# Performance work log

Hardware: AMD Instinct MI355X
Metric: run time of the kernel (lower is better)

Reference implementation:

```python
import jax, jax.numpy as jnp
import numpy as np

S, B, I, H = 2048, 4096, 2, 6  # seq, batch, input_size, hidden_size


def setup_inputs() -> dict:
    key = jax.random.key(0)
    ks = jax.random.split(key, 11)
    init = lambda k, sh: jax.random.normal(k, sh, dtype=jnp.float32) * 0.1
    return {
        "x": jax.random.normal(ks[0], (S, B, I), dtype=jnp.float32),
        # layer-0 LSTM params (PyTorch gate order: i, f, g, o)
        "Wih0": init(ks[1], (4 * H, I)),
        "Whh0": init(ks[2], (4 * H, H)),
        "bih0": init(ks[3], (4 * H,)),
        "bhh0": init(ks[4], (4 * H,)),
        # layer-1 LSTM params
        "Wih1": init(ks[5], (4 * H, H)),
        "Whh1": init(ks[6], (4 * H, H)),
        "bih1": init(ks[7], (4 * H,)),
        "bhh1": init(ks[8], (4 * H,)),
        # final Linear(6, 1)
        "W2": init(ks[9], (1, H)),
        "b2": init(ks[10], (1,)),
    }


def _lstm_layer(x, Wih, Whh, bih, bhh):
    # x: (S, B, in_dim) -> hidden outputs (S, B, H)
    Bn = x.shape[1]
    Hn = Whh.shape[1]
    b = bih + bhh
    # precompute input projections for all timesteps at once (memory-bound GEMM)
    xg = jnp.einsum("sbi,gi->sbg", x, Wih) + b  # (S, B, 4H)

    def step(carry, xt_g):
        h, c = carry
        g = xt_g + h @ Whh.T  # (B, 4H)
        i, f, gg, o = jnp.split(g, 4, axis=-1)
        i = jax.nn.sigmoid(i)
        f = jax.nn.sigmoid(f)
        gg = jnp.tanh(gg)
        o = jax.nn.sigmoid(o)
        c = f * c + i * gg
        h = o * jnp.tanh(c)
        return (h, c), h

    h0 = jnp.zeros((Bn, Hn), dtype=x.dtype)
    c0 = jnp.zeros((Bn, Hn), dtype=x.dtype)
    _, hs = jax.lax.scan(step, (h0, c0), xg)
    return hs  # (S, B, H)


def reference(x, Wih0, Whh0, bih0, bhh0, Wih1, Whh1, bih1, bhh1, W2, b2):
    h1 = _lstm_layer(x, Wih0, Whh0, bih0, bhh0)   # (S, B, H)
    h2 = _lstm_layer(h1, Wih1, Whh1, bih1, bhh1)  # (S, B, H); dropout disabled (eval)
    flat = h2.reshape(-1, H)                       # (S*B, H)
    out = flat @ W2.T + b2                         # (S*B, 1) — original discards final view
    return out
```

## Files before the change

kernel.cpp:

```cpp
#include <hip/hip_runtime.h>

#define SEQ   2048
#define BATCH 4096
#define HID   6
#define BLK   256

typedef float v2f __attribute__((ext_vector_type(2)));
typedef unsigned u2 __attribute__((ext_vector_type(2)));

__device__ __forceinline__ float fexp2(float a) {
#if __has_builtin(__builtin_amdgcn_exp2f)
  return __builtin_amdgcn_exp2f(a);
#else
  float r; asm("v_exp_f32 %0, %1" : "=v"(r) : "v"(a)); return r;
#endif
}
__device__ __forceinline__ float frcp(float a) {
#if __has_builtin(__builtin_amdgcn_rcpf)
  return __builtin_amdgcn_rcpf(a);
#else
  float r; asm("v_rcp_f32 %0, %1" : "=v"(r) : "v"(a)); return r;
#endif
}

template <int CTRL>
__device__ __forceinline__ float dppf(float v) {
  int r = __builtin_amdgcn_update_dpp(0, __builtin_bit_cast(int, v), CTRL, 0xF, 0xF, true);
  return __builtin_bit_cast(float, r);
}

template <int OFF>
__device__ __forceinline__ float swzf(float v) {
  int r = __builtin_amdgcn_ds_swizzle(__builtin_bit_cast(int, v), OFF);
  return __builtin_bit_cast(float, r);
}
#define BC0 0x18
#define BC1 0x38
#define BC2 0x58
#define BC3 0x78
#define BC4 0x98
#define BC5 0xB8

__device__ __forceinline__ float xor16f(float v, bool hi) {
#if __has_builtin(__builtin_amdgcn_permlane16_swap)
  u2 r = __builtin_amdgcn_permlane16_swap(__builtin_bit_cast(unsigned, v),
                                          __builtin_bit_cast(unsigned, v), false, false);
  return __builtin_bit_cast(float, hi ? r.x : r.y);
#else
  unsigned d = __builtin_bit_cast(unsigned, v), s = d;
  asm volatile("v_permlane16_swap_b32 %0, %1" : "+v"(d), "+v"(s));
  return __builtin_bit_cast(float, hi ? d : s);
#endif
}

__global__ __launch_bounds__(BLK, 2) void lstm2_kernel(
    const float* __restrict__ x,
    const float* __restrict__ Wih0, const float* __restrict__ Whh0,
    const float* __restrict__ bih0, const float* __restrict__ bhh0,
    const float* __restrict__ Wih1, const float* __restrict__ Whh1,
    const float* __restrict__ bih1, const float* __restrict__ bhh1,
    const float* __restrict__ W2,   const float* __restrict__ b2,
    float* __restrict__ out)
{
  __shared__ float obuf[64][8];

  const int tid = threadIdx.x;
  const int wib = tid >> 6;
  const int l6  = tid & 63;
  const int el  = l6 >> 5;
  const int r5  = l6 & 31;
  const bool hiL = (r5 & 16) != 0;
  const int p   = (r5 >> 3) & 1;
  const int u   = r5 & 7;
  const int uu  = (u < HID) ? u : (HID - 1);
  const int b   = blockIdx.x * 8 + wib * 2 + el;

  const int r0 = p ? (2 * HID + uu) : uu;
  const int r1 = p ? (3 * HID + uu) : (HID + uu);
  const float A  = p ? 2.f : 1.f;
  const float Bc = p ? -1.f : 0.f;
  const float K0 = p ? -2.8853900817779268f : -1.4426950408889634f;
  const float K1 = -1.4426950408889634f;
  const float KT =  2.8853900817779268f;

  v2f WA0[3], WA1[3], WB0[3], WB1[3];
  float BS0, BS1;
  if (!hiL) {
    WA0[0] = v2f{K0 * Wih0[r0 * 2 + 0], K0 * Wih0[r0 * 2 + 1]};
    WA1[0] = v2f{K1 * Wih0[r1 * 2 + 0], K1 * Wih0[r1 * 2 + 1]};
    WA0[1] = v2f{0.f, 0.f}; WA0[2] = v2f{0.f, 0.f};
    WA1[1] = v2f{0.f, 0.f}; WA1[2] = v2f{0.f, 0.f};
#pragma unroll
    for (int k = 0; k < 3; ++k) {
      WB0[k] = v2f{K0 * Whh0[r0 * HID + 2 * k], K0 * Whh0[r0 * HID + 2 * k + 1]};
      WB1[k] = v2f{K1 * Whh0[r1 * HID + 2 * k], K1 * Whh0[r1 * HID + 2 * k + 1]};
    }
    BS0 = K0 * (bih0[r0] + bhh0[r0]);
    BS1 = K1 * (bih0[r1] + bhh0[r1]);
  } else {
#pragma unroll
    for (int k = 0; k < 3; ++k) {
      WA0[k] = v2f{K0 * Wih1[r0 * HID + 2 * k], K0 * Wih1[r0 * HID + 2 * k + 1]};
      WA1[k] = v2f{K1 * Wih1[r1 * HID + 2 * k], K1 * Wih1[r1 * HID + 2 * k + 1]};
      WB0[k] = v2f{K0 * Whh1[r0 * HID + 2 * k], K0 * Whh1[r0 * HID + 2 * k + 1]};
      WB1[k] = v2f{K1 * Whh1[r1 * HID + 2 * k], K1 * Whh1[r1 * HID + 2 * k + 1]};
    }
    BS0 = K0 * (bih1[r0] + bhh1[r0]);
    BS1 = K1 * (bih1[r1] + bhh1[r1]);
  }
  const v2f w2p0 = v2f{W2[0], W2[1]}, w2p1 = v2f{W2[2], W2[3]}, w2p2 = v2f{W2[4], W2[5]};
  const float bout = b2[0];

  float h = 0.f, c = 0.f;

  auto gath = [&](float hv, v2f (&g)[3]) {
    g[0] = v2f{swzf<BC0>(hv), swzf<BC1>(hv)};
    g[1] = v2f{swzf<BC2>(hv), swzf<BC3>(hv)};
    g[2] = v2f{swzf<BC4>(hv), swzf<BC5>(hv)};
  };

  auto step = [&](v2f xc, float& ov) {
    v2f g2[3]; gath(h, g2);
    float hs = xor16f(h, hiL);
    v2f g1[3]; gath(hs, g1);
    v2f v10 = hiL ? g1[0] : xc;

    v2f a0v = __builtin_elementwise_fma(WA0[0], v10, v2f{BS0, 0.f});
    a0v = __builtin_elementwise_fma(WA0[1], g1[1], a0v);
    a0v = __builtin_elementwise_fma(WA0[2], g1[2], a0v);
    a0v = __builtin_elementwise_fma(WB0[0], g2[0], a0v);
    a0v = __builtin_elementwise_fma(WB0[1], g2[1], a0v);
    a0v = __builtin_elementwise_fma(WB0[2], g2[2], a0v);
    float a0 = a0v.x + a0v.y;

    v2f a1v = __builtin_elementwise_fma(WA1[0], v10, v2f{BS1, 0.f});
    a1v = __builtin_elementwise_fma(WA1[1], g1[1], a1v);
    a1v = __builtin_elementwise_fma(WA1[2], g1[2], a1v);
    a1v = __builtin_elementwise_fma(WB1[0], g2[0], a1v);
    a1v = __builtin_elementwise_fma(WB1[1], g2[1], a1v);
    a1v = __builtin_elementwise_fma(WB1[2], g2[2], a1v);
    float a1 = a1v.x + a1v.y;

    v2f ao = __builtin_elementwise_fma(w2p0, g2[0],
             __builtin_elementwise_fma(w2p1, g2[1],
             __builtin_elementwise_fma(w2p2, g2[2], v2f{bout, 0.f})));
    ov = ao.x + ao.y;

    float g0  = fmaf(A, frcp(1.f + fexp2(a0)), Bc);
    float g1v = frcp(1.f + fexp2(a1));
    float xg0 = dppf<0x128>(g0);
    float xg1 = dppf<0x128>(g1v);
    float m = g0 * xg0;
    float f = p ? xg1 : g1v;
    float o = p ? g1v : xg1;
    c = fmaf(f, c, m);
    float th = fmaf(-2.f, frcp(1.f + fexp2(c * KT)), 1.f);
    h = o * th;
  };

  auto flush = [&](int rbase) {
    const int r = tid >> 2, jj = (tid & 3) * 2;
    float2 vv = *(const float2*)&obuf[r][jj];
    *(float2*)&out[(size_t)(rbase + r) * BATCH + blockIdx.x * 8 + jj] = vv;
  };

  const v2f* x2 = (const v2f*)x;
  v2f xc  = x2[(size_t)0 * BATCH + b];
  v2f xn1 = x2[(size_t)1 * BATCH + b];
  v2f xn2 = x2[(size_t)2 * BATCH + b];
  v2f xn3 = x2[(size_t)3 * BATCH + b];

  {
    float ov;
    step(xc, ov);
    if (hiL) { h = 0.f; c = 0.f; }
    v2f xf = x2[(size_t)4 * BATCH + b];
    xc = xn1; xn1 = xn2; xn2 = xn3; xn3 = xf;
  }

#pragma unroll 1
  for (int t = 1; t < SEQ; ++t) {
    int tf = t + 4; tf = (tf < SEQ) ? tf : (SEQ - 1);
    v2f xf = x2[(size_t)tf * BATCH + b];

    float ov;
    step(xc, ov);

    if (t >= 2) {
      const int r = t - 2;
      if (hiL && p == 0 && u == 0) obuf[r & 63][wib * 2 + el] = ov;
      if ((r & 63) == 63) {
        __syncthreads();
        flush(r - 63);
        __syncthreads();
      }
    }
    xc = xn1; xn1 = xn2; xn2 = xn3; xn3 = xf;
  }

  {
    float ov;
    step(xc, ov);
    if (hiL && p == 0 && u == 0) obuf[62][wib * 2 + el] = ov;
    v2f g2[3]; gath(h, g2);
    v2f ao = __builtin_elementwise_fma(w2p0, g2[0],
             __builtin_elementwise_fma(w2p1, g2[1],
             __builtin_elementwise_fma(w2p2, g2[2], v2f{bout, 0.f})));
    if (hiL && p == 0 && u == 0) obuf[63][wib * 2 + el] = ao.x + ao.y;
    __syncthreads();
    flush(SEQ - 64);
  }
}

extern "C" void kernel_launch(void* const* d_in, const int* in_sizes, int n_in,
                              void* d_out, int out_size, void* d_ws, size_t ws_size,
                              hipStream_t stream) {
  const float* x    = (const float*)d_in[0];
  const float* Wih0 = (const float*)d_in[1];
  const float* Whh0 = (const float*)d_in[2];
  const float* bih0 = (const float*)d_in[3];
  const float* bhh0 = (const float*)d_in[4];
  const float* Wih1 = (const float*)d_in[5];
  const float* Whh1 = (const float*)d_in[6];
  const float* bih1 = (const float*)d_in[7];
  const float* bhh1 = (const float*)d_in[8];
  const float* W2   = (const float*)d_in[9];
  const float* b2   = (const float*)d_in[10];
  float* out = (float*)d_out;

  dim3 grid(BATCH / 8);
  dim3 block(BLK);
  hipLaunchKernelGGL(lstm2_kernel, grid, block, 0, stream,
                     x, Wih0, Whh0, bih0, bhh0, Wih1, Whh1, bih1, bhh1, W2, b2, out);
}
```

Measured before the change: 669.0 us.

## Interleave two independent batch chains per lane to hide swizzle latency

Result: slower. 844.1 us (+26.2%).

```diff
diff --git a/kernel.cpp b/kernel.cpp
--- a/kernel.cpp
+++ b/kernel.cpp
@@ -53,7 +53,13 @@
 #endif
 }
 
-__global__ __launch_bounds__(BLK, 2) void lstm2_kernel(
+__device__ __forceinline__ void schedbar() {
+#if __has_builtin(__builtin_amdgcn_sched_barrier)
+  __builtin_amdgcn_sched_barrier(0);
+#endif
+}
+
+__global__ __launch_bounds__(BLK, 1) void lstm2_kernel(
     const float* __restrict__ x,
     const float* __restrict__ Wih0, const float* __restrict__ Whh0,
     const float* __restrict__ bih0, const float* __restrict__ bhh0,
@@ -62,18 +68,20 @@
     const float* __restrict__ W2,   const float* __restrict__ b2,
     float* __restrict__ out)
 {
-  __shared__ float obuf[64][8];
+  __shared__ float obuf[64][16];
 
   const int tid = threadIdx.x;
   const int wib = tid >> 6;
   const int l6  = tid & 63;
-  const int el  = l6 >> 5;
-  const int r5  = l6 & 31;
-  const bool hiL = (r5 & 16) != 0;
-  const int p   = (r5 >> 3) & 1;
-  const int u   = r5 & 7;
+  const int e5  = l6 >> 5;
+  const bool hiL = (l6 & 16) != 0;
+  const int p   = (l6 >> 3) & 1;
+  const int u   = l6 & 7;
   const int uu  = (u < HID) ? u : (HID - 1);
-  const int b   = blockIdx.x * 8 + wib * 2 + el;
+  const int elA = wib * 4 + e5;
+  const int elB = elA + 2;
+  const int bA  = blockIdx.x * 16 + elA;
+  const int bB  = bA + 2;
 
   const int r0 = p ? (2 * HID + uu) : uu;
   const int r1 = p ? (3 * HID + uu) : (HID + uu);
@@ -111,7 +119,8 @@
   const v2f w2p0 = v2f{W2[0], W2[1]}, w2p1 = v2f{W2[2], W2[3]}, w2p2 = v2f{W2[4], W2[5]};
   const float bout = b2[0];
 
-  float h = 0.f, c = 0.f;
+  float hA = 0.f, cA = 0.f, hB = 0.f, cB = 0.f;
+  v2f gA2[3] = {}, gA1[3] = {}, gB2[3] = {}, gB1[3] = {};
 
   auto gath = [&](float hv, v2f (&g)[3]) {
     g[0] = v2f{swzf<BC0>(hv), swzf<BC1>(hv)};
@@ -119,12 +128,9 @@
     g[2] = v2f{swzf<BC4>(hv), swzf<BC5>(hv)};
   };
 
-  auto step = [&](v2f xc, float& ov) {
-    v2f g2[3]; gath(h, g2);
-    float hs = xor16f(h, hiL);
-    v2f g1[3]; gath(hs, g1);
+  auto compute = [&](float& h, float& c, const v2f (&g2)[3], const v2f (&g1)[3],
+                     v2f xc, float& ov) {
     v2f v10 = hiL ? g1[0] : xc;
-
     v2f a0v = __builtin_elementwise_fma(WA0[0], v10, v2f{BS0, 0.f});
     a0v = __builtin_elementwise_fma(WA0[1], g1[1], a0v);
     a0v = __builtin_elementwise_fma(WA0[2], g1[2], a0v);
@@ -158,55 +164,79 @@
     h = o * th;
   };
 
+  auto issue = [&](float h, v2f (&g2)[3], v2f (&g1)[3]) {
+    gath(h, g2);
+    float hs = xor16f(h, hiL);
+    gath(hs, g1);
+  };
+
   auto flush = [&](int rbase) {
-    const int r = tid >> 2, jj = (tid & 3) * 2;
-    float2 vv = *(const float2*)&obuf[r][jj];
-    *(float2*)&out[(size_t)(rbase + r) * BATCH + blockIdx.x * 8 + jj] = vv;
+    const int r = tid >> 2, jj = (tid & 3) * 4;
+    float4 vv = *(const float4*)&obuf[r][jj];
+    *(float4*)&out[(size_t)(rbase + r) * BATCH + blockIdx.x * 16 + jj] = vv;
   };
 
   const v2f* x2 = (const v2f*)x;
-  v2f xc  = x2[(size_t)0 * BATCH + b];
-  v2f xn1 = x2[(size_t)1 * BATCH + b];
-  v2f xn2 = x2[(size_t)2 * BATCH + b];
-  v2f xn3 = x2[(size_t)3 * BATCH + b];
+  v2f xcA = x2[(size_t)0 * BATCH + bA], xcB = x2[(size_t)0 * BATCH + bB];
+  v2f n1A = x2[(size_t)1 * BATCH + bA], n1B = x2[(size_t)1 * BATCH + bB];
+  v2f n2A = x2[(size_t)2 * BATCH + bA], n2B = x2[(size_t)2 * BATCH + bB];
+  v2f n3A = x2[(size_t)3 * BATCH + bA], n3B = x2[(size_t)3 * BATCH + bB];
 
   {
     float ov;
-    step(xc, ov);
-    if (hiL) { h = 0.f; c = 0.f; }
-    v2f xf = x2[(size_t)4 * BATCH + b];
-    xc = xn1; xn1 = xn2; xn2 = xn3; xn3 = xf;
+    compute(hA, cA, gA2, gA1, xcA, ov);
+    compute(hB, cB, gB2, gB1, xcB, ov);
+    if (hiL) { hA = 0.f; cA = 0.f; hB = 0.f; cB = 0.f; }
+    issue(hA, gA2, gA1);
+    issue(hB, gB2, gB1);
+    v2f fA = x2[(size_t)4 * BATCH + bA], fB = x2[(size_t)4 * BATCH + bB];
+    xcA = n1A; n1A = n2A; n2A = n3A; n3A = fA;
+    xcB = n1B; n1B = n2B; n2B = n3B; n3B = fB;
   }
 
 #pragma unroll 1
   for (int t = 1; t < SEQ; ++t) {
     int tf = t + 4; tf = (tf < SEQ) ? tf : (SEQ - 1);
-    v2f xf = x2[(size_t)tf * BATCH + b];
-
-    float ov;
-    step(xc, ov);
-
-    if (t >= 2) {
-      const int r = t - 2;
-      if (hiL && p == 0 && u == 0) obuf[r & 63][wib * 2 + el] = ov;
-      if ((r & 63) == 63) {
-        __syncthreads();
-        flush(r - 63);
-        __syncthreads();
-      }
-    }
-    xc = xn1; xn1 = xn2; xn2 = xn3; xn3 = xf;
+    v2f fA = x2[(size_t)tf * BATCH + bA];
+    v2f fB = x2[(size_t)tf * BATCH + bB];
+
+    float ovA, ovB;
+    compute(hA, cA, gA2, gA1, xcA, ovA);
+    if (t >= 2 && hiL && p == 0 && u == 0) obuf[(t - 2) & 63][elA] = ovA;
+    issue(hA, gA2, gA1);
+    schedbar();
+
+    compute(hB, cB, gB2, gB1, xcB, ovB);
+    if (t >= 2 && hiL && p == 0 && u == 0) obuf[(t - 2) & 63][elB] = ovB;
+    issue(hB, gB2, gB1);
+    schedbar();
+
+    if (t >= 2 && ((t - 2) & 63) == 63) {
+      __syncthreads();
+      flush(t - 2 - 63);
+      __syncthreads();
+    }
+    xcA = n1A; n1A = n2A; n2A = n3A; n3A = fA;
+    xcB = n1B; n1B = n2B; n2B = n3B; n3B = fB;
   }
 
   {
-    float ov;
-    step(xc, ov);
-    if (hiL && p == 0 && u == 0) obuf[62][wib * 2 + el] = ov;
-    v2f g2[3]; gath(h, g2);
-    v2f ao = __builtin_elementwise_fma(w2p0, g2[0],
-             __builtin_elementwise_fma(w2p1, g2[1],
-             __builtin_elementwise_fma(w2p2, g2[2], v2f{bout, 0.f})));
-    if (hiL && p == 0 && u == 0) obuf[63][wib * 2 + el] = ao.x + ao.y;
+    float ovA, ovB;
+    compute(hA, cA, gA2, gA1, xcA, ovA);
+    compute(hB, cB, gB2, gB1, xcB, ovB);
+    if (hiL && p == 0 && u == 0) { obuf[62][elA] = ovA; obuf[62][elB] = ovB; }
+    gath(hA, gA2);
+    gath(hB, gB2);
+    v2f aoA = __builtin_elementwise_fma(w2p0, gA2[0],
+              __builtin_elementwise_fma(w2p1, gA2[1],
+              __builtin_elementwise_fma(w2p2, gA2[2], v2f{bout, 0.f})));
+    v2f aoB = __builtin_elementwise_fma(w2p0, gB2[0],
+              __builtin_elementwise_fma(w2p1, gB2[1],
+              __builtin_elementwise_fma(w2p2, gB2[2], v2f{bout, 0.f})));
+    if (hiL && p == 0 && u == 0) {
+      obuf[63][elA] = aoA.x + aoA.y;
+      obuf[63][elB] = aoB.x + aoB.y;
+    }
     __syncthreads();
     flush(SEQ - 64);
   }
@@ -228,7 +258,7 @@
   const float* b2   = (const float*)d_in[10];
   float* out = (float*)d_out;
 
-  dim3 grid(BATCH / 8);
+  dim3 grid(BATCH / 16);
   dim3 block(BLK);
   hipLaunchKernelGGL(lstm2_kernel, grid, block, 0, stream,
                      x, Wih0, Whh0, bih0, bhh0, Wih1, Whh1, bih1, bhh1, W2, b2, out);
```
